# Optimization experiments

Hardware: AMD Instinct MI355X
Metric: run time of the kernel (lower is better)

Reference implementation:

```python
import jax, jax.numpy as jnp
import numpy as np

BS, D, L, H = 8, 256, 1024, 8
DK = D // H
EPS = 1e-8


def setup_inputs() -> dict:
    key = jax.random.key(0)
    ks = jax.random.split(key, 9)
    queries = jax.random.normal(ks[0], (BS, D, L), jnp.float32)
    keys = jax.random.normal(ks[1], (BS, D, L), jnp.float32)
    values = jax.random.normal(ks[2], (BS, D, L), jnp.float32)
    # binary float mask over positions, (bs, L, 1) as the module expects
    mask = (jax.random.uniform(ks[3], (BS, L, 1)) > 0.1).astype(jnp.float32)
    # grouped 1x1 conv weights: one (dk, dk) block per head (xavier-ish scale)
    wscale = np.sqrt(2.0 / (DK + DK)).astype(np.float32)
    Wq = jax.random.normal(ks[4], (H, DK, DK), jnp.float32) * wscale
    Wk = jax.random.normal(ks[5], (H, DK, DK), jnp.float32) * wscale
    Wv = jax.random.normal(ks[6], (H, DK, DK), jnp.float32) * wscale
    # full 1x1 conv projection
    Wp = jax.random.normal(ks[7], (D, D), jnp.float32) * np.sqrt(1.0 / D).astype(np.float32)
    bp = jnp.zeros((D,), jnp.float32)
    return {"queries": queries, "keys": keys, "values": values, "mask": mask,
            "Wq": Wq, "Wk": Wk, "Wv": Wv, "Wp": Wp, "bp": bp}


def _grouped_conv1x1(x, W):
    # x: (bs, D, L) viewed as (bs, H, dk, L); W: (H, dk_out, dk_in)
    bs, _, l = x.shape
    xh = x.reshape(bs, H, DK, l)
    return jnp.einsum('hij,bhjl->bhil', W, xh)  # (bs, H, dk, L)


def _masked_softmax(logits, mask4):
    # logits: (bs, H, L, L); mask4: (bs, 1, 1, L) -- faithful to module's custom softmax
    max_value = jax.lax.stop_gradient(jnp.max(logits * mask4, axis=-1, keepdims=True))
    z = (logits - max_value) * mask4
    m = jnp.exp(z) * mask4
    n = jnp.sum(m, axis=-1, keepdims=True)
    p_mask = mask4 * jnp.swapaxes(mask4, 2, 3)  # (bs, 1, L, L)
    return p_mask * (m / (n + EPS))


def reference(queries, keys, values, mask, Wq, Wk, Wv, Wp, bp):
    bs, c, l = queries.shape
    m = jnp.swapaxes(mask, 1, 2)          # (bs, 1, L)
    m4 = m[:, :, None, :]                  # (bs, 1, 1, L)
    q = _grouped_conv1x1(queries, Wq) * m4  # (bs, H, dk, L)
    k = _grouped_conv1x1(keys, Wk) * m4
    v = _grouped_conv1x1(values, Wv)
    # attn[b,h,d,e] = sum_c q[b,h,c,d] k[b,h,c,e]  (no 1/sqrt(dk) scaling, as in source)
    attn = jnp.einsum('bhcd,bhce->bhde', q, k)
    atn = _masked_softmax(attn, m4)
    # value[b,h,c,k] = sum_d atn[b,h,k,d] * (v*mask)[b,h,c,d]
    val = jnp.einsum('bhkd,bhcd->bhck', atn, v * m4)
    val = val.reshape(bs, c, l)
    out = jnp.einsum('ij,bjl->bil', Wp, val) + bp[None, :, None]
    return jnp.swapaxes(out * m, 1, 2)      # (bs, L, D)
```

## Files before the change

### kernel.cpp

```cpp
#include <hip/hip_runtime.h>
#include <math.h>


constexpr int cD  = 256;
constexpr int cL  = 1024;
constexpr int cH  = 8;
constexpr int cDK = 32;

typedef _Float16 f16;
typedef __attribute__((ext_vector_type(8))) _Float16 h8;
typedef __attribute__((ext_vector_type(4))) _Float16 h4;
typedef __attribute__((ext_vector_type(4))) float f4v;

__global__ __launch_bounds__(256, 4) void proj_kv_kernel(
    const float* __restrict__ keys, const float* __restrict__ values,
    const float* __restrict__ mask, const float* __restrict__ Wk,
    const float* __restrict__ Wv, f16* __restrict__ kp_h,
    f16* __restrict__ vp_h)
{
    __shared__ __align__(16) float xs[32][68];
    __shared__ __align__(16) float wT[32][36];
    __shared__ float msl[64];

    const int t   = threadIdx.x;
    const int bid = blockIdx.x;
    const int lt  = bid & 15;
    const int h   = (bid >> 4) & 7;
    const int b   = bid >> 7;
    const int l0  = lt * 64;

    if (t < 64) msl[t] = mask[b * cL + l0 + t];

    for (int idx = t; idx < 512; idx += 256) {
        int j = idx >> 4, l4 = (idx & 15) * 4;
        *reinterpret_cast<float4*>(&xs[j][l4]) =
            *reinterpret_cast<const float4*>(&keys[(b * cD + h * cDK + j) * cL + l0 + l4]);
    }
    for (int idx = t; idx < 1024; idx += 256) {
        int c = idx >> 5, j = idx & 31;
        wT[j][c] = Wk[(h * cDK + c) * cDK + j];
    }
    __syncthreads();
    {
        const int l = t >> 2, ig = t & 3;
        float acc[8] = {0, 0, 0, 0, 0, 0, 0, 0};
        #pragma unroll
        for (int j = 0; j < 32; ++j) {
            float xv = xs[j][l];
            float4 w0 = *reinterpret_cast<const float4*>(&wT[j][ig * 8]);
            float4 w1 = *reinterpret_cast<const float4*>(&wT[j][ig * 8 + 4]);
            acc[0] += w0.x * xv; acc[1] += w0.y * xv;
            acc[2] += w0.z * xv; acc[3] += w0.w * xv;
            acc[4] += w1.x * xv; acc[5] += w1.y * xv;
            acc[6] += w1.z * xv; acc[7] += w1.w * xv;
        }
        float mk = msl[l];
        h8 hv;
        #pragma unroll
        for (int i = 0; i < 8; ++i) hv[i] = (f16)(acc[i] * mk);
        size_t off = (((size_t)(b * cH + h)) * cL + l0 + l) * cDK + ig * 8;
        *reinterpret_cast<h8*>(&kp_h[off]) = hv;
    }
    __syncthreads();

    for (int idx = t; idx < 512; idx += 256) {
        int j = idx >> 4, l4 = (idx & 15) * 4;
        *reinterpret_cast<float4*>(&xs[j][l4]) =
            *reinterpret_cast<const float4*>(&values[(b * cD + h * cDK + j) * cL + l0 + l4]);
    }
    for (int idx = t; idx < 1024; idx += 256) {
        int c = idx >> 5, j = idx & 31;
        wT[j][c] = Wv[(h * cDK + c) * cDK + j];
    }
    __syncthreads();
    {
        const int l4 = (t & 15) * 4;
        const int c0 = (t >> 4) * 2;
        float a0[4] = {0, 0, 0, 0}, a1[4] = {0, 0, 0, 0};
        #pragma unroll
        for (int j = 0; j < 32; ++j) {
            float4 xv = *reinterpret_cast<const float4*>(&xs[j][l4]);
            float w0 = wT[j][c0], w1 = wT[j][c0 + 1];
            a0[0] += w0 * xv.x; a0[1] += w0 * xv.y; a0[2] += w0 * xv.z; a0[3] += w0 * xv.w;
            a1[0] += w1 * xv.x; a1[1] += w1 * xv.y; a1[2] += w1 * xv.z; a1[3] += w1 * xv.w;
        }
        size_t base = ((size_t)(b * cH + h)) * cDK;
        h4 v0, v1;
        #pragma unroll
        for (int i = 0; i < 4; ++i) { v0[i] = (f16)a0[i]; v1[i] = (f16)a1[i]; }
        *reinterpret_cast<h4*>(&vp_h[(base + c0) * cL + l0 + l4])     = v0;
        *reinterpret_cast<h4*>(&vp_h[(base + c0 + 1) * cL + l0 + l4]) = v1;
    }
}

__global__ __launch_bounds__(256, 4) void attn_kernel(
    const float* __restrict__ queries, const float* __restrict__ mask,
    const float* __restrict__ Wq, const f16* __restrict__ kp_h,
    const f16* __restrict__ vp_h, f16* __restrict__ val_h)
{
    __shared__ __align__(16) char smem[37888];
    f16*   ks    = (f16*)smem;
    f16*   vsb   = (f16*)(smem + 10240);
    f16*   qsb   = (f16*)(smem + 19456);
    f16*   pbf   = (f16*)(smem + 24576);
    float* msall = (float*)(smem + 33792);
    float* qtmp  = (float*)smem;
    float* wqt   = (float*)(smem + 8704);

    const int t     = threadIdx.x;
    const int bid   = blockIdx.x;
    const int strip = bid & 15;
    const int h     = (bid >> 4) & 7;
    const int b     = bid >> 7;
    const int r0    = strip * 64;
    const int lane  = t & 63;
    const int w     = t >> 6;
    const int ln15  = lane & 15;
    const int lq    = lane >> 4;

    {
        int j = t >> 3, f8 = (t & 7) * 8;
        const float* src = &queries[(b * cD + h * cDK + j) * cL + r0 + f8];
        float4 v0 = *reinterpret_cast<const float4*>(src);
        float4 v1 = *reinterpret_cast<const float4*>(src + 4);
        *reinterpret_cast<float4*>(&qtmp[j * 68 + f8])     = v0;
        *reinterpret_cast<float4*>(&qtmp[j * 68 + f8 + 4]) = v1;
    }
    {
        int c = t >> 3, j4 = (t & 7) * 4;
        float4 wv = *reinterpret_cast<const float4*>(&Wq[(h * cDK + c) * cDK + j4]);
        wqt[(j4 + 0) * 32 + c] = wv.x; wqt[(j4 + 1) * 32 + c] = wv.y;
        wqt[(j4 + 2) * 32 + c] = wv.z; wqt[(j4 + 3) * 32 + c] = wv.w;
    }
    *reinterpret_cast<float4*>(&msall[t * 4]) =
        *reinterpret_cast<const float4*>(&mask[b * cL + t * 4]);
    __syncthreads();

    {
        float acc[8] = {0, 0, 0, 0, 0, 0, 0, 0};
        #pragma unroll
        for (int j = 0; j < 32; ++j) {
            float xv = qtmp[j * 68 + lane];
            float4 w0 = *reinterpret_cast<const float4*>(&wqt[j * 32 + w * 8]);
            float4 w1 = *reinterpret_cast<const float4*>(&wqt[j * 32 + w * 8 + 4]);
            acc[0] += w0.x * xv; acc[1] += w0.y * xv;
            acc[2] += w0.z * xv; acc[3] += w0.w * xv;
            acc[4] += w1.x * xv; acc[5] += w1.y * xv;
            acc[6] += w1.z * xv; acc[7] += w1.w * xv;
        }
        h8 hv;
        #pragma unroll
        for (int i = 0; i < 8; ++i) hv[i] = (f16)acc[i];
        *reinterpret_cast<h8*>(&qsb[lane * 40 + w * 8]) = hv;
    }
    __syncthreads();

    const size_t kvbase = ((size_t)(b * cH + h)) * 32768;
    const int se = t >> 2, sb = (t & 3) * 8;
    const int vc = t >> 3, veb = (t & 7) * 8;

    {
        h8 kh = *reinterpret_cast<const h8*>(&kp_h[kvbase + se * 32 + sb]);
        *reinterpret_cast<h8*>(&ks[se * 40 + sb]) = kh;
        h8 vv = *reinterpret_cast<const h8*>(&vp_h[kvbase + vc * 1024 + veb]);
        *reinterpret_cast<h8*>(&vsb[vc * 72 + veb]) = vv;
    }

    const h8 qf = *reinterpret_cast<const h8*>(&qsb[(w * 16 + ln15) * 40 + lq * 8]);

    f4v o0 = {0.f, 0.f, 0.f, 0.f}, o1 = {0.f, 0.f, 0.f, 0.f};
    float mo = -INFINITY, lr = 0.f;
    const int prow  = (w * 16 + ln15) * 72;
    const int vsoff = ln15 * 72 + lq * 8;

    for (int et = 0; et < 16; ++et) {
        __syncthreads();
        const int pp = et & 1;
        const bool pre = (et < 15);
        h8 khp, vvp;
        if (pre) {
            const int e0n = (et + 1) * 64;
            khp = *reinterpret_cast<const h8*>(&kp_h[kvbase + (e0n + se) * 32 + sb]);
            vvp = *reinterpret_cast<const h8*>(&vp_h[kvbase + vc * 1024 + e0n + veb]);
        }

        f4v sA[4];
        #pragma unroll
        for (int es = 0; es < 4; ++es) {
            const h8 kf = *reinterpret_cast<const h8*>(
                &ks[pp * 2560 + (es * 16 + ln15) * 40 + lq * 8]);
            f4v z = {0.f, 0.f, 0.f, 0.f};
            sA[es] = __builtin_amdgcn_mfma_f32_16x16x32_f16(kf, qf, z, 0, 0, 0);
        }

        float tm = fmaxf(fmaxf(fmaxf(sA[0][0], sA[0][1]), fmaxf(sA[0][2], sA[0][3])),
                   fmaxf(fmaxf(fmaxf(sA[1][0], sA[1][1]), fmaxf(sA[1][2], sA[1][3])),
                   fmaxf(fmaxf(fmaxf(sA[2][0], sA[2][1]), fmaxf(sA[2][2], sA[2][3])),
                         fmaxf(fmaxf(sA[3][0], sA[3][1]), fmaxf(sA[3][2], sA[3][3])))));
        tm = fmaxf(tm, __shfl_xor(tm, 16));
        tm = fmaxf(tm, __shfl_xor(tm, 32));
        const float mn = fmaxf(mo, tm);
        const float al = __expf(mo - mn);
        mo = mn;
        o0[0] *= al; o0[1] *= al; o0[2] *= al; o0[3] *= al;
        o1[0] *= al; o1[1] *= al; o1[2] *= al; o1[3] *= al;

        float ps = 0.f;
        #pragma unroll
        for (int es = 0; es < 4; ++es) {
            float4 mk4 = *reinterpret_cast<const float4*>(&msall[et * 64 + es * 16 + lq * 4]);
            float p0 = __expf((sA[es][0] - mn) * mk4.x) * mk4.x;
            float p1 = __expf((sA[es][1] - mn) * mk4.y) * mk4.y;
            float p2 = __expf((sA[es][2] - mn) * mk4.z) * mk4.z;
            float p3 = __expf((sA[es][3] - mn) * mk4.w) * mk4.w;
            ps += (p0 + p1) + (p2 + p3);
            h4 pk; pk[0] = (f16)p0; pk[1] = (f16)p1; pk[2] = (f16)p2; pk[3] = (f16)p3;
            *reinterpret_cast<h4*>(&pbf[prow + es * 16 + lq * 4]) = pk;
        }
        ps += __shfl_xor(ps, 16);
        ps += __shfl_xor(ps, 32);
        lr = lr * al + ps;

        #pragma unroll
        for (int ch = 0; ch < 2; ++ch) {
            h8 pf  = *reinterpret_cast<const h8*>(&pbf[prow + ch * 32 + lq * 8]);
            h8 va0 = *reinterpret_cast<const h8*>(&vsb[pp * 2304 + vsoff + ch * 32]);
            h8 va1 = *reinterpret_cast<const h8*>(&vsb[pp * 2304 + vsoff + ch * 32 + 1152]);
            o0 = __builtin_amdgcn_mfma_f32_16x16x32_f16(va0, pf, o0, 0, 0, 0);
            o1 = __builtin_amdgcn_mfma_f32_16x16x32_f16(va1, pf, o1, 0, 0, 0);
        }

        if (pre) {
            *reinterpret_cast<h8*>(&ks[(pp ^ 1) * 2560 + se * 40 + sb]) = khp;
            *reinterpret_cast<h8*>(&vsb[(pp ^ 1) * 2304 + vc * 72 + veb]) = vvp;
        }
    }

    {
        const float linv = 1.0f / (lr + 1e-8f);
        const size_t obase = ((size_t)(b * cL + r0 + w * 16 + ln15)) * cD + h * cDK;
        h4 q0, q1;
        #pragma unroll
        for (int i = 0; i < 4; ++i) {
            q0[i] = (f16)(o0[i] * linv);
            q1[i] = (f16)(o1[i] * linv);
        }
        *reinterpret_cast<h4*>(&val_h[obase + lq * 4])      = q0;
        *reinterpret_cast<h4*>(&val_h[obase + 16 + lq * 4]) = q1;
    }
}

__global__ __launch_bounds__(256, 2) void outproj_kernel(
    const f16* __restrict__ val_h, const float* __restrict__ Wp,
    const float* __restrict__ bp, const float* __restrict__ mask,
    float* __restrict__ out)
{
    __shared__ __align__(16) f16 vt[64 * 264];
    __shared__ __align__(16) f16 wpb[64 * 264];
    __shared__ float mrow[64];

    const int t    = threadIdx.x;
    const int bid  = blockIdx.x;
    const int it   = bid & 3;
    const int lt   = (bid >> 2) & 15;
    const int b    = bid >> 6;
    const int l0   = lt * 64, i0 = it * 64;
    const int lane = t & 63, w = t >> 6, ln15 = lane & 15, lq = lane >> 4;

    {
        int row = t & 63, seg = (t >> 6) * 64;
        const f16* src = &val_h[((size_t)(b * cL + l0 + row)) * cD + seg];
        #pragma unroll
        for (int k = 0; k < 8; ++k)
            *reinterpret_cast<h8*>(&vt[row * 264 + seg + k * 8]) =
                *reinterpret_cast<const h8*>(src + k * 8);
    }
    {
        int row = t & 63, seg = (t >> 6) * 64;
        const float* src = &Wp[((size_t)(i0 + row)) * cD + seg];
        #pragma unroll
        for (int k = 0; k < 8; ++k) {
            float4 f0 = *reinterpret_cast<const float4*>(src + k * 8);
            float4 f1 = *reinterpret_cast<const float4*>(src + k * 8 + 4);
            h8 hv;
            hv[0] = (f16)f0.x; hv[1] = (f16)f0.y; hv[2] = (f16)f0.z; hv[3] = (f16)f0.w;
            hv[4] = (f16)f1.x; hv[5] = (f16)f1.y; hv[6] = (f16)f1.z; hv[7] = (f16)f1.w;
            *reinterpret_cast<h8*>(&wpb[row * 264 + seg + k * 8]) = hv;
        }
    }
    if (t < 64) mrow[t] = mask[b * cL + l0 + t];
    __syncthreads();

    f4v acc[4] = {{0.f, 0.f, 0.f, 0.f}, {0.f, 0.f, 0.f, 0.f},
                  {0.f, 0.f, 0.f, 0.f}, {0.f, 0.f, 0.f, 0.f}};
    #pragma unroll
    for (int kc = 0; kc < 8; ++kc) {
        h8 aA = *reinterpret_cast<const h8*>(&vt[(w * 16 + ln15) * 264 + kc * 32 + lq * 8]);
        #pragma unroll
        for (int ti = 0; ti < 4; ++ti) {
            h8 bB = *reinterpret_cast<const h8*>(&wpb[(ti * 16 + ln15) * 264 + kc * 32 + lq * 8]);
            acc[ti] = __builtin_amdgcn_mfma_f32_16x16x32_f16(aA, bB, acc[ti], 0, 0, 0);
        }
    }

    float mk[4];
    #pragma unroll
    for (int rg = 0; rg < 4; ++rg) mk[rg] = mrow[w * 16 + lq * 4 + rg];
    #pragma unroll
    for (int ti = 0; ti < 4; ++ti) {
        float bpv = bp[i0 + ti * 16 + ln15];
        #pragma unroll
        for (int rg = 0; rg < 4; ++rg) {
            int l = l0 + w * 16 + lq * 4 + rg;
            out[((size_t)(b * cL + l)) * cD + i0 + ti * 16 + ln15] =
                (acc[ti][rg] + bpv) * mk[rg];
        }
    }
}

extern "C" void kernel_launch(void* const* d_in, const int* in_sizes, int n_in,
                              void* d_out, int out_size, void* d_ws, size_t ws_size,
                              hipStream_t stream) {
    const float* queries = (const float*)d_in[0];
    const float* keys    = (const float*)d_in[1];
    const float* values  = (const float*)d_in[2];
    const float* mask    = (const float*)d_in[3];
    const float* Wq      = (const float*)d_in[4];
    const float* Wk      = (const float*)d_in[5];
    const float* Wv      = (const float*)d_in[6];
    const float* Wp      = (const float*)d_in[7];
    const float* bp      = (const float*)d_in[8];
    float* out = (float*)d_out;

    char* wsb = (char*)d_ws;
    f16* kp_h  = (f16*)(wsb);
    f16* vp_h  = (f16*)(wsb + (4u << 20));
    f16* val_h = (f16*)(wsb + (8u << 20));

    proj_kv_kernel<<<dim3(1024), dim3(256), 0, stream>>>(keys, values, mask, Wk, Wv,
                                                         kp_h, vp_h);
    attn_kernel<<<dim3(1024), dim3(256), 0, stream>>>(queries, mask, Wq,
                                                      kp_h, vp_h, val_h);
    outproj_kernel<<<dim3(512), dim3(256), 0, stream>>>(val_h, Wp, bp, mask, out);
}
```

Before: 131.7 us.

## Process two 16-row query tiles per wave to reuse K/V shared-memory tiles

Each attention block now covers 128 query rows instead of 64, and each wave runs two 16-row tiles. Every K and V fragment read from shared memory feeds twice as many MFMAs, and each K/V tile is loaded once per 128 rows instead of per 64. This halves the grid to 512 blocks, raises shared memory and register use, and lowers launch bounds to 2 blocks per CU. The block index order also changes so consecutive blocks cover different batch-head pairs rather than different strips of the same one.

After: 134.2 us. Within noise of the previous version (+1.9%).

```diff
diff --git a/kernel.cpp b/kernel.cpp
--- a/kernel.cpp
+++ b/kernel.cpp
@@ -93,38 +93,36 @@
     }
 }
 
-__global__ __launch_bounds__(256, 4) void attn_kernel(
+__global__ __launch_bounds__(256, 2) void attn_kernel(
     const float* __restrict__ queries, const float* __restrict__ mask,
     const float* __restrict__ Wq, const f16* __restrict__ kp_h,
     const f16* __restrict__ vp_h, f16* __restrict__ val_h)
 {
-    __shared__ __align__(16) char smem[37888];
+    __shared__ __align__(16) char smem[52224];
     f16*   ks    = (f16*)smem;
     f16*   vsb   = (f16*)(smem + 10240);
     f16*   qsb   = (f16*)(smem + 19456);
-    f16*   pbf   = (f16*)(smem + 24576);
-    float* msall = (float*)(smem + 33792);
-    float* qtmp  = (float*)smem;
-    float* wqt   = (float*)(smem + 8704);
+    f16*   pbf   = (f16*)(smem + 29696);
+    float* msall = (float*)(smem + 48128);
+    float* wqt   = (float*)smem;
+    float* qtmp  = (float*)(smem + 29696);
 
     const int t     = threadIdx.x;
     const int bid   = blockIdx.x;
-    const int strip = bid & 15;
-    const int h     = (bid >> 4) & 7;
-    const int b     = bid >> 7;
-    const int r0    = strip * 64;
+    const int bh    = bid & 63;
+    const int strip = bid >> 6;
+    const int b     = bh >> 3;
+    const int h     = bh & 7;
+    const int r0    = strip * 128;
     const int lane  = t & 63;
     const int w     = t >> 6;
     const int ln15  = lane & 15;
     const int lq    = lane >> 4;
 
-    {
-        int j = t >> 3, f8 = (t & 7) * 8;
-        const float* src = &queries[(b * cD + h * cDK + j) * cL + r0 + f8];
-        float4 v0 = *reinterpret_cast<const float4*>(src);
-        float4 v1 = *reinterpret_cast<const float4*>(src + 4);
-        *reinterpret_cast<float4*>(&qtmp[j * 68 + f8])     = v0;
-        *reinterpret_cast<float4*>(&qtmp[j * 68 + f8 + 4]) = v1;
+    for (int idx = t; idx < 1024; idx += 256) {
+        int j = idx >> 5, l4 = (idx & 31) * 4;
+        *reinterpret_cast<float4*>(&qtmp[j * 132 + l4]) =
+            *reinterpret_cast<const float4*>(&queries[(b * cD + h * cDK + j) * cL + r0 + l4]);
     }
     {
         int c = t >> 3, j4 = (t & 7) * 4;
@@ -136,11 +134,13 @@
         *reinterpret_cast<const float4*>(&mask[b * cL + t * 4]);
     __syncthreads();
 
-    {
+    #pragma unroll
+    for (int rr = 0; rr < 2; ++rr) {
+        const int r = rr * 64 + lane;
         float acc[8] = {0, 0, 0, 0, 0, 0, 0, 0};
         #pragma unroll
         for (int j = 0; j < 32; ++j) {
-            float xv = qtmp[j * 68 + lane];
+            float xv = qtmp[j * 132 + r];
             float4 w0 = *reinterpret_cast<const float4*>(&wqt[j * 32 + w * 8]);
             float4 w1 = *reinterpret_cast<const float4*>(&wqt[j * 32 + w * 8 + 4]);
             acc[0] += w0.x * xv; acc[1] += w0.y * xv;
@@ -151,11 +151,11 @@
         h8 hv;
         #pragma unroll
         for (int i = 0; i < 8; ++i) hv[i] = (f16)acc[i];
-        *reinterpret_cast<h8*>(&qsb[lane * 40 + w * 8]) = hv;
-    }
-    __syncthreads();
-
-    const size_t kvbase = ((size_t)(b * cH + h)) * 32768;
+        *reinterpret_cast<h8*>(&qsb[r * 40 + w * 8]) = hv;
+    }
+    __syncthreads();
+
+    const size_t kvbase = ((size_t)bh) * 32768;
     const int se = t >> 2, sb = (t & 3) * 8;
     const int vc = t >> 3, veb = (t & 7) * 8;
 
@@ -166,12 +166,15 @@
         *reinterpret_cast<h8*>(&vsb[vc * 72 + veb]) = vv;
     }
 
-    const h8 qf = *reinterpret_cast<const h8*>(&qsb[(w * 16 + ln15) * 40 + lq * 8]);
-
-    f4v o0 = {0.f, 0.f, 0.f, 0.f}, o1 = {0.f, 0.f, 0.f, 0.f};
-    float mo = -INFINITY, lr = 0.f;
-    const int prow  = (w * 16 + ln15) * 72;
-    const int vsoff = ln15 * 72 + lq * 8;
+    const h8 qf0 = *reinterpret_cast<const h8*>(&qsb[(w * 32 + ln15) * 40 + lq * 8]);
+    const h8 qf1 = *reinterpret_cast<const h8*>(&qsb[(w * 32 + 16 + ln15) * 40 + lq * 8]);
+
+    f4v o[2][2] = {{{0.f, 0.f, 0.f, 0.f}, {0.f, 0.f, 0.f, 0.f}},
+                   {{0.f, 0.f, 0.f, 0.f}, {0.f, 0.f, 0.f, 0.f}}};
+    float mo[2] = {-INFINITY, -INFINITY};
+    float lr[2] = {0.f, 0.f};
+    const int prow0 = (w * 32 + ln15) * 72;
+    const int prow1 = (w * 32 + 16 + ln15) * 72;
 
     for (int et = 0; et < 16; ++et) {
         __syncthreads();
@@ -184,50 +187,70 @@
             vvp = *reinterpret_cast<const h8*>(&vp_h[kvbase + vc * 1024 + e0n + veb]);
         }
 
-        f4v sA[4];
+        f4v sA[4][2];
         #pragma unroll
         for (int es = 0; es < 4; ++es) {
             const h8 kf = *reinterpret_cast<const h8*>(
                 &ks[pp * 2560 + (es * 16 + ln15) * 40 + lq * 8]);
-            f4v z = {0.f, 0.f, 0.f, 0.f};
-            sA[es] = __builtin_amdgcn_mfma_f32_16x16x32_f16(kf, qf, z, 0, 0, 0);
-        }
-
-        float tm = fmaxf(fmaxf(fmaxf(sA[0][0], sA[0][1]), fmaxf(sA[0][2], sA[0][3])),
-                   fmaxf(fmaxf(fmaxf(sA[1][0], sA[1][1]), fmaxf(sA[1][2], sA[1][3])),
-                   fmaxf(fmaxf(fmaxf(sA[2][0], sA[2][1]), fmaxf(sA[2][2], sA[2][3])),
-                         fmaxf(fmaxf(sA[3][0], sA[3][1]), fmaxf(sA[3][2], sA[3][3])))));
-        tm = fmaxf(tm, __shfl_xor(tm, 16));
-        tm = fmaxf(tm, __shfl_xor(tm, 32));
-        const float mn = fmaxf(mo, tm);
-        const float al = __expf(mo - mn);
-        mo = mn;
-        o0[0] *= al; o0[1] *= al; o0[2] *= al; o0[3] *= al;
-        o1[0] *= al; o1[1] *= al; o1[2] *= al; o1[3] *= al;
-
-        float ps = 0.f;
+            f4v z0 = {0.f, 0.f, 0.f, 0.f}, z1 = {0.f, 0.f, 0.f, 0.f};
+            sA[es][0] = __builtin_amdgcn_mfma_f32_16x16x32_f16(kf, qf0, z0, 0, 0, 0);
+            sA[es][1] = __builtin_amdgcn_mfma_f32_16x16x32_f16(kf, qf1, z1, 0, 0, 0);
+        }
+
+        float mn[2], al[2];
+        #pragma unroll
+        for (int rt = 0; rt < 2; ++rt) {
+            float tm = fmaxf(
+                fmaxf(fmaxf(sA[0][rt][0], sA[0][rt][1]), fmaxf(sA[0][rt][2], sA[0][rt][3])),
+                fmaxf(fmaxf(fmaxf(sA[1][rt][0], sA[1][rt][1]), fmaxf(sA[1][rt][2], sA[1][rt][3])),
+                fmaxf(fmaxf(fmaxf(sA[2][rt][0], sA[2][rt][1]), fmaxf(sA[2][rt][2], sA[2][rt][3])),
+                      fmaxf(fmaxf(sA[3][rt][0], sA[3][rt][1]), fmaxf(sA[3][rt][2], sA[3][rt][3])))));
+            tm = fmaxf(tm, __shfl_xor(tm, 16));
+            tm = fmaxf(tm, __shfl_xor(tm, 32));
+            mn[rt] = fmaxf(mo[rt], tm);
+            al[rt] = __expf(mo[rt] - mn[rt]);
+            mo[rt] = mn[rt];
+            #pragma unroll
+            for (int ch = 0; ch < 2; ++ch) {
+                o[rt][ch][0] *= al[rt]; o[rt][ch][1] *= al[rt];
+                o[rt][ch][2] *= al[rt]; o[rt][ch][3] *= al[rt];
+            }
+        }
+
+        float ps[2] = {0.f, 0.f};
         #pragma unroll
         for (int es = 0; es < 4; ++es) {
             float4 mk4 = *reinterpret_cast<const float4*>(&msall[et * 64 + es * 16 + lq * 4]);
-            float p0 = __expf((sA[es][0] - mn) * mk4.x) * mk4.x;
-            float p1 = __expf((sA[es][1] - mn) * mk4.y) * mk4.y;
-            float p2 = __expf((sA[es][2] - mn) * mk4.z) * mk4.z;
-            float p3 = __expf((sA[es][3] - mn) * mk4.w) * mk4.w;
-            ps += (p0 + p1) + (p2 + p3);
-            h4 pk; pk[0] = (f16)p0; pk[1] = (f16)p1; pk[2] = (f16)p2; pk[3] = (f16)p3;
-            *reinterpret_cast<h4*>(&pbf[prow + es * 16 + lq * 4]) = pk;
-        }
-        ps += __shfl_xor(ps, 16);
-        ps += __shfl_xor(ps, 32);
-        lr = lr * al + ps;
+            #pragma unroll
+            for (int rt = 0; rt < 2; ++rt) {
+                float p0 = __expf((sA[es][rt][0] - mn[rt]) * mk4.x) * mk4.x;
+                float p1 = __expf((sA[es][rt][1] - mn[rt]) * mk4.y) * mk4.y;
+                float p2 = __expf((sA[es][rt][2] - mn[rt]) * mk4.z) * mk4.z;
+                float p3 = __expf((sA[es][rt][3] - mn[rt]) * mk4.w) * mk4.w;
+                ps[rt] += (p0 + p1) + (p2 + p3);
+                h4 pk; pk[0] = (f16)p0; pk[1] = (f16)p1; pk[2] = (f16)p2; pk[3] = (f16)p3;
+                const int prow = rt ? prow1 : prow0;
+                *reinterpret_cast<h4*>(&pbf[prow + es * 16 + lq * 4]) = pk;
+            }
+        }
+        #pragma unroll
+        for (int rt = 0; rt < 2; ++rt) {
+            float p = ps[rt];
+            p += __shfl_xor(p, 16);
+            p += __shfl_xor(p, 32);
+            lr[rt] = lr[rt] * al[rt] + p;
+        }
 
         #pragma unroll
         for (int ch = 0; ch < 2; ++ch) {
-            h8 pf  = *reinterpret_cast<const h8*>(&pbf[prow + ch * 32 + lq * 8]);
-            h8 va0 = *reinterpret_cast<const h8*>(&vsb[pp * 2304 + vsoff + ch * 32]);
-            h8 va1 = *reinterpret_cast<const h8*>(&vsb[pp * 2304 + vsoff + ch * 32 + 1152]);
-            o0 = __builtin_amdgcn_mfma_f32_16x16x32_f16(va0, pf, o0, 0, 0, 0);
-            o1 = __builtin_amdgcn_mfma_f32_16x16x32_f16(va1, pf, o1, 0, 0, 0);
+            h8 pf0 = *reinterpret_cast<const h8*>(&pbf[prow0 + ch * 32 + lq * 8]);
+            h8 pf1 = *reinterpret_cast<const h8*>(&pbf[prow1 + ch * 32 + lq * 8]);
+            h8 va0 = *reinterpret_cast<const h8*>(&vsb[pp * 2304 + ln15 * 72 + ch * 32 + lq * 8]);
+            h8 va1 = *reinterpret_cast<const h8*>(&vsb[pp * 2304 + (16 + ln15) * 72 + ch * 32 + lq * 8]);
+            o[0][0] = __builtin_amdgcn_mfma_f32_16x16x32_f16(va0, pf0, o[0][0], 0, 0, 0);
+            o[0][1] = __builtin_amdgcn_mfma_f32_16x16x32_f16(va1, pf0, o[0][1], 0, 0, 0);
+            o[1][0] = __builtin_amdgcn_mfma_f32_16x16x32_f16(va0, pf1, o[1][0], 0, 0, 0);
+            o[1][1] = __builtin_amdgcn_mfma_f32_16x16x32_f16(va1, pf1, o[1][1], 0, 0, 0);
         }
 
         if (pre) {
@@ -236,14 +259,16 @@
         }
     }
 
-    {
-        const float linv = 1.0f / (lr + 1e-8f);
-        const size_t obase = ((size_t)(b * cL + r0 + w * 16 + ln15)) * cD + h * cDK;
+    #pragma unroll
+    for (int rt = 0; rt < 2; ++rt) {
+        const float linv = 1.0f / (lr[rt] + 1e-8f);
+        const int r = r0 + w * 32 + rt * 16 + ln15;
+        const size_t obase = ((size_t)(b * cL + r)) * cD + h * cDK;
         h4 q0, q1;
         #pragma unroll
         for (int i = 0; i < 4; ++i) {
-            q0[i] = (f16)(o0[i] * linv);
-            q1[i] = (f16)(o1[i] * linv);
+            q0[i] = (f16)(o[rt][0][i] * linv);
+            q1[i] = (f16)(o[rt][1][i] * linv);
         }
         *reinterpret_cast<h4*>(&val_h[obase + lq * 4])      = q0;
         *reinterpret_cast<h4*>(&val_h[obase + 16 + lq * 4]) = q1;
@@ -339,7 +364,7 @@
 
     proj_kv_kernel<<<dim3(1024), dim3(256), 0, stream>>>(keys, values, mask, Wk, Wv,
                                                          kp_h, vp_h);
-    attn_kernel<<<dim3(1024), dim3(256), 0, stream>>>(queries, mask, Wq,
-                                                      kp_h, vp_h, val_h);
+    attn_kernel<<<dim3(512), dim3(256), 0, stream>>>(queries, mask, Wq,
+                                                     kp_h, vp_h, val_h);
     outproj_kernel<<<dim3(512), dim3(256), 0, stream>>>(val_h, Wp, bp, mask, out);
 }
```

## Move Q projection into MFMA-based QKV projection kernel and slim attention smem

Applied to the files above, without the earlier changes.

Q, K and V projections now run in a single pre-kernel that uses MFMA f16 instructions instead of scalar FMA loops through shared memory. Q is written to workspace in f16, so the attention kernel drops its Q projection prologue, its q/mask shared buffers and a sync, and raises its occupancy hint. Mask values are read directly from global memory each tile, and the row-sum shuffle reduction moves out of the loop to the end. The trade-offs are an extra Q round trip through memory, f16 rounding of inputs and weights before projection, and strided scalar global loads and stores in the projection kernel.

Result: faster. 127.3 us (-3.3%).

```diff
diff --git a/kernel.cpp b/kernel.cpp
--- a/kernel.cpp
+++ b/kernel.cpp
@@ -12,152 +12,105 @@
 typedef __attribute__((ext_vector_type(4))) _Float16 h4;
 typedef __attribute__((ext_vector_type(4))) float f4v;
 
-__global__ __launch_bounds__(256, 4) void proj_kv_kernel(
-    const float* __restrict__ keys, const float* __restrict__ values,
-    const float* __restrict__ mask, const float* __restrict__ Wk,
-    const float* __restrict__ Wv, f16* __restrict__ kp_h,
-    f16* __restrict__ vp_h)
+__global__ __launch_bounds__(256, 4) void proj_qkv_kernel(
+    const float* __restrict__ queries, const float* __restrict__ keys,
+    const float* __restrict__ values, const float* __restrict__ mask,
+    const float* __restrict__ Wq, const float* __restrict__ Wk,
+    const float* __restrict__ Wv, f16* __restrict__ qp_h,
+    f16* __restrict__ kp_h, f16* __restrict__ vp_h)
 {
-    __shared__ __align__(16) float xs[32][68];
-    __shared__ __align__(16) float wT[32][36];
-    __shared__ float msl[64];
-
-    const int t   = threadIdx.x;
-    const int bid = blockIdx.x;
-    const int lt  = bid & 15;
-    const int h   = (bid >> 4) & 7;
-    const int b   = bid >> 7;
-    const int l0  = lt * 64;
-
-    if (t < 64) msl[t] = mask[b * cL + l0 + t];
-
-    for (int idx = t; idx < 512; idx += 256) {
-        int j = idx >> 4, l4 = (idx & 15) * 4;
-        *reinterpret_cast<float4*>(&xs[j][l4]) =
-            *reinterpret_cast<const float4*>(&keys[(b * cD + h * cDK + j) * cL + l0 + l4]);
-    }
-    for (int idx = t; idx < 1024; idx += 256) {
-        int c = idx >> 5, j = idx & 31;
-        wT[j][c] = Wk[(h * cDK + c) * cDK + j];
-    }
-    __syncthreads();
-    {
-        const int l = t >> 2, ig = t & 3;
-        float acc[8] = {0, 0, 0, 0, 0, 0, 0, 0};
-        #pragma unroll
-        for (int j = 0; j < 32; ++j) {
-            float xv = xs[j][l];
-            float4 w0 = *reinterpret_cast<const float4*>(&wT[j][ig * 8]);
-            float4 w1 = *reinterpret_cast<const float4*>(&wT[j][ig * 8 + 4]);
-            acc[0] += w0.x * xv; acc[1] += w0.y * xv;
-            acc[2] += w0.z * xv; acc[3] += w0.w * xv;
-            acc[4] += w1.x * xv; acc[5] += w1.y * xv;
-            acc[6] += w1.z * xv; acc[7] += w1.w * xv;
-        }
-        float mk = msl[l];
-        h8 hv;
-        #pragma unroll
-        for (int i = 0; i < 8; ++i) hv[i] = (f16)(acc[i] * mk);
-        size_t off = (((size_t)(b * cH + h)) * cL + l0 + l) * cDK + ig * 8;
-        *reinterpret_cast<h8*>(&kp_h[off]) = hv;
-    }
-    __syncthreads();
-
-    for (int idx = t; idx < 512; idx += 256) {
-        int j = idx >> 4, l4 = (idx & 15) * 4;
-        *reinterpret_cast<float4*>(&xs[j][l4]) =
-            *reinterpret_cast<const float4*>(&values[(b * cD + h * cDK + j) * cL + l0 + l4]);
-    }
-    for (int idx = t; idx < 1024; idx += 256) {
-        int c = idx >> 5, j = idx & 31;
-        wT[j][c] = Wv[(h * cDK + c) * cDK + j];
-    }
-    __syncthreads();
-    {
-        const int l4 = (t & 15) * 4;
-        const int c0 = (t >> 4) * 2;
-        float a0[4] = {0, 0, 0, 0}, a1[4] = {0, 0, 0, 0};
-        #pragma unroll
-        for (int j = 0; j < 32; ++j) {
-            float4 xv = *reinterpret_cast<const float4*>(&xs[j][l4]);
-            float w0 = wT[j][c0], w1 = wT[j][c0 + 1];
-            a0[0] += w0 * xv.x; a0[1] += w0 * xv.y; a0[2] += w0 * xv.z; a0[3] += w0 * xv.w;
-            a1[0] += w1 * xv.x; a1[1] += w1 * xv.y; a1[2] += w1 * xv.z; a1[3] += w1 * xv.w;
-        }
-        size_t base = ((size_t)(b * cH + h)) * cDK;
-        h4 v0, v1;
-        #pragma unroll
-        for (int i = 0; i < 4; ++i) { v0[i] = (f16)a0[i]; v1[i] = (f16)a1[i]; }
-        *reinterpret_cast<h4*>(&vp_h[(base + c0) * cL + l0 + l4])     = v0;
-        *reinterpret_cast<h4*>(&vp_h[(base + c0 + 1) * cL + l0 + l4]) = v1;
+    const int t    = threadIdx.x;
+    const int bid  = blockIdx.x;
+    const int lt   = bid & 15;
+    const int bh   = bid >> 4;
+    const int h    = bh & 7;
+    const int b    = bh >> 3;
+    const int l0   = lt * 64;
+    const int lane = t & 63, w = t >> 6, ln15 = lane & 15, lq = lane >> 4;
+    const int l    = l0 + w * 16 + ln15;
+
+    const float mk = mask[b * cL + l];
+    const size_t xbase = ((size_t)(b * cD + h * cDK)) * cL + l;
+    const int    wbase = h * cDK * cDK + lq * 8;
+
+    const float* Xs[3] = {queries, keys, values};
+    const float* Ws[3] = {Wq, Wk, Wv};
+    f4v d0[3], d1[3];
+
+    #pragma unroll
+    for (int m = 0; m < 3; ++m) {
+        const float* __restrict__ X = Xs[m];
+        const float* __restrict__ W = Ws[m];
+        h8 bx, a0, a1;
+        #pragma unroll
+        for (int i = 0; i < 8; ++i)
+            bx[i] = (f16)X[xbase + (size_t)(lq * 8 + i) * cL];
+        #pragma unroll
+        for (int i = 0; i < 8; ++i) {
+            a0[i] = (f16)W[wbase + ln15 * cDK + i];
+            a1[i] = (f16)W[wbase + (16 + ln15) * cDK + i];
+        }
+        f4v z = {0.f, 0.f, 0.f, 0.f};
+        d0[m] = __builtin_amdgcn_mfma_f32_16x16x32_f16(a0, bx, z, 0, 0, 0);
+        d1[m] = __builtin_amdgcn_mfma_f32_16x16x32_f16(a1, bx, z, 0, 0, 0);
+    }
+
+    {
+        const size_t qb = ((size_t)bh * cL + l) * cDK;
+        h4 o0, o1;
+        #pragma unroll
+        for (int i = 0; i < 4; ++i) { o0[i] = (f16)d0[0][i]; o1[i] = (f16)d1[0][i]; }
+        *reinterpret_cast<h4*>(&qp_h[qb + lq * 4])      = o0;
+        *reinterpret_cast<h4*>(&qp_h[qb + 16 + lq * 4]) = o1;
+    }
+    {
+        const size_t kb = ((size_t)bh * cL + l) * cDK;
+        h4 o0, o1;
+        #pragma unroll
+        for (int i = 0; i < 4; ++i) {
+            o0[i] = (f16)(d0[1][i] * mk);
+            o1[i] = (f16)(d1[1][i] * mk);
+        }
+        *reinterpret_cast<h4*>(&kp_h[kb + lq * 4])      = o0;
+        *reinterpret_cast<h4*>(&kp_h[kb + 16 + lq * 4]) = o1;
+    }
+    {
+        const size_t vb = (size_t)bh * cDK * cL + l;
+        #pragma unroll
+        for (int i = 0; i < 4; ++i) {
+            vp_h[vb + (size_t)(lq * 4 + i) * cL]      = (f16)d0[2][i];
+            vp_h[vb + (size_t)(16 + lq * 4 + i) * cL] = (f16)d1[2][i];
+        }
     }
 }
 
-__global__ __launch_bounds__(256, 4) void attn_kernel(
-    const float* __restrict__ queries, const float* __restrict__ mask,
-    const float* __restrict__ Wq, const f16* __restrict__ kp_h,
-    const f16* __restrict__ vp_h, f16* __restrict__ val_h)
+__global__ __launch_bounds__(256, 5) void attn_kernel(
+    const float* __restrict__ mask, const f16* __restrict__ qp_h,
+    const f16* __restrict__ kp_h, const f16* __restrict__ vp_h,
+    f16* __restrict__ val_h)
 {
-    __shared__ __align__(16) char smem[37888];
-    f16*   ks    = (f16*)smem;
-    f16*   vsb   = (f16*)(smem + 10240);
-    f16*   qsb   = (f16*)(smem + 19456);
-    f16*   pbf   = (f16*)(smem + 24576);
-    float* msall = (float*)(smem + 33792);
-    float* qtmp  = (float*)smem;
-    float* wqt   = (float*)(smem + 8704);
+    __shared__ __align__(16) char smem[28672];
+    f16* ks  = (f16*)smem;
+    f16* vsb = (f16*)(smem + 10240);
+    f16* pbf = (f16*)(smem + 19456);
 
     const int t     = threadIdx.x;
     const int bid   = blockIdx.x;
     const int strip = bid & 15;
-    const int h     = (bid >> 4) & 7;
-    const int b     = bid >> 7;
+    const int bh    = bid >> 4;
+    const int b     = bh >> 3;
     const int r0    = strip * 64;
     const int lane  = t & 63;
     const int w     = t >> 6;
     const int ln15  = lane & 15;
     const int lq    = lane >> 4;
 
-    {
-        int j = t >> 3, f8 = (t & 7) * 8;
-        const float* src = &queries[(b * cD + h * cDK + j) * cL + r0 + f8];
-        float4 v0 = *reinterpret_cast<const float4*>(src);
-        float4 v1 = *reinterpret_cast<const float4*>(src + 4);
-        *reinterpret_cast<float4*>(&qtmp[j * 68 + f8])     = v0;
-        *reinterpret_cast<float4*>(&qtmp[j * 68 + f8 + 4]) = v1;
-    }
-    {
-        int c = t >> 3, j4 = (t & 7) * 4;
-        float4 wv = *reinterpret_cast<const float4*>(&Wq[(h * cDK + c) * cDK + j4]);
-        wqt[(j4 + 0) * 32 + c] = wv.x; wqt[(j4 + 1) * 32 + c] = wv.y;
-        wqt[(j4 + 2) * 32 + c] = wv.z; wqt[(j4 + 3) * 32 + c] = wv.w;
-    }
-    *reinterpret_cast<float4*>(&msall[t * 4]) =
-        *reinterpret_cast<const float4*>(&mask[b * cL + t * 4]);
-    __syncthreads();
-
-    {
-        float acc[8] = {0, 0, 0, 0, 0, 0, 0, 0};
-        #pragma unroll
-        for (int j = 0; j < 32; ++j) {
-            float xv = qtmp[j * 68 + lane];
-            float4 w0 = *reinterpret_cast<const float4*>(&wqt[j * 32 + w * 8]);
-            float4 w1 = *reinterpret_cast<const float4*>(&wqt[j * 32 + w * 8 + 4]);
-            acc[0] += w0.x * xv; acc[1] += w0.y * xv;
-            acc[2] += w0.z * xv; acc[3] += w0.w * xv;
-            acc[4] += w1.x * xv; acc[5] += w1.y * xv;
-            acc[6] += w1.z * xv; acc[7] += w1.w * xv;
-        }
-        h8 hv;
-        #pragma unroll
-        for (int i = 0; i < 8; ++i) hv[i] = (f16)acc[i];
-        *reinterpret_cast<h8*>(&qsb[lane * 40 + w * 8]) = hv;
-    }
-    __syncthreads();
-
-    const size_t kvbase = ((size_t)(b * cH + h)) * 32768;
+    const size_t kvbase = ((size_t)bh) * 32768;
     const int se = t >> 2, sb = (t & 3) * 8;
     const int vc = t >> 3, veb = (t & 7) * 8;
+
+    const h8 qf = *reinterpret_cast<const h8*>(
+        &qp_h[((size_t)bh * cL + r0 + w * 16 + ln15) * cDK + lq * 8]);
 
     {
         h8 kh = *reinterpret_cast<const h8*>(&kp_h[kvbase + se * 32 + sb]);
@@ -166,10 +119,8 @@
         *reinterpret_cast<h8*>(&vsb[vc * 72 + veb]) = vv;
     }
 
-    const h8 qf = *reinterpret_cast<const h8*>(&qsb[(w * 16 + ln15) * 40 + lq * 8]);
-
     f4v o0 = {0.f, 0.f, 0.f, 0.f}, o1 = {0.f, 0.f, 0.f, 0.f};
-    float mo = -INFINITY, lr = 0.f;
+    float mo = -INFINITY, lrp = 0.f;
     const int prow  = (w * 16 + ln15) * 72;
     const int vsoff = ln15 * 72 + lq * 8;
 
@@ -183,6 +134,11 @@
             khp = *reinterpret_cast<const h8*>(&kp_h[kvbase + (e0n + se) * 32 + sb]);
             vvp = *reinterpret_cast<const h8*>(&vp_h[kvbase + vc * 1024 + e0n + veb]);
         }
+        float4 mk4[4];
+        #pragma unroll
+        for (int es = 0; es < 4; ++es)
+            mk4[es] = *reinterpret_cast<const float4*>(
+                &mask[b * cL + et * 64 + es * 16 + lq * 4]);
 
         f4v sA[4];
         #pragma unroll
@@ -208,18 +164,15 @@
         float ps = 0.f;
         #pragma unroll
         for (int es = 0; es < 4; ++es) {
-            float4 mk4 = *reinterpret_cast<const float4*>(&msall[et * 64 + es * 16 + lq * 4]);
-            float p0 = __expf((sA[es][0] - mn) * mk4.x) * mk4.x;
-            float p1 = __expf((sA[es][1] - mn) * mk4.y) * mk4.y;
-            float p2 = __expf((sA[es][2] - mn) * mk4.z) * mk4.z;
-            float p3 = __expf((sA[es][3] - mn) * mk4.w) * mk4.w;
+            float p0 = mk4[es].x * __expf(sA[es][0] - mn);
+            float p1 = mk4[es].y * __expf(sA[es][1] - mn);
+            float p2 = mk4[es].z * __expf(sA[es][2] - mn);
+            float p3 = mk4[es].w * __expf(sA[es][3] - mn);
             ps += (p0 + p1) + (p2 + p3);
             h4 pk; pk[0] = (f16)p0; pk[1] = (f16)p1; pk[2] = (f16)p2; pk[3] = (f16)p3;
             *reinterpret_cast<h4*>(&pbf[prow + es * 16 + lq * 4]) = pk;
         }
-        ps += __shfl_xor(ps, 16);
-        ps += __shfl_xor(ps, 32);
-        lr = lr * al + ps;
+        lrp = lrp * al + ps;
 
         #pragma unroll
         for (int ch = 0; ch < 2; ++ch) {
@@ -237,7 +190,11 @@
     }
 
     {
+        float lr = lrp;
+        lr += __shfl_xor(lr, 16);
+        lr += __shfl_xor(lr, 32);
         const float linv = 1.0f / (lr + 1e-8f);
+        const int h = bh & 7;
         const size_t obase = ((size_t)(b * cL + r0 + w * 16 + ln15)) * cD + h * cDK;
         h4 q0, q1;
         #pragma unroll
@@ -333,13 +290,14 @@
     float* out = (float*)d_out;
 
     char* wsb = (char*)d_ws;
-    f16* kp_h  = (f16*)(wsb);
-    f16* vp_h  = (f16*)(wsb + (4u << 20));
-    f16* val_h = (f16*)(wsb + (8u << 20));
-
-    proj_kv_kernel<<<dim3(1024), dim3(256), 0, stream>>>(keys, values, mask, Wk, Wv,
-                                                         kp_h, vp_h);
-    attn_kernel<<<dim3(1024), dim3(256), 0, stream>>>(queries, mask, Wq,
-                                                      kp_h, vp_h, val_h);
+    f16* qp_h  = (f16*)(wsb);
+    f16* kp_h  = (f16*)(wsb + (4u << 20));
+    f16* vp_h  = (f16*)(wsb + (8u << 20));
+    f16* val_h = (f16*)(wsb + (12u << 20));
+
+    proj_qkv_kernel<<<dim3(1024), dim3(256), 0, stream>>>(
+        queries, keys, values, mask, Wq, Wk, Wv, qp_h, kp_h, vp_h);
+    attn_kernel<<<dim3(1024), dim3(256), 0, stream>>>(
+        mask, qp_h, kp_h, vp_h, val_h);
     outproj_kernel<<<dim3(512), dim3(256), 0, stream>>>(val_h, Wp, bp, mask, out);
 }
```
